# Kernel tuning notes

Hardware: AMD Instinct MI355X
Metric: run time of the kernel (lower is better)

Reference implementation:

```python
import jax, jax.numpy as jnp
import numpy as np


def _rel_pos_table(size, rel_pos):
    # q_size == k_size, fixed_input_size=True -> no interpolation, lambda=1
    coords = jnp.arange(size)[:, None] - jnp.arange(size)[None, :] + (size - 1)
    return rel_pos[coords]  # (size, size, head_dim)


def setup_inputs() -> dict:
    key = jax.random.key(0)
    ks = jax.random.split(key, 7)
    N, H, W, C = 8, 32, 32, 768
    hd = C // 12
    return {
        "x": jax.random.normal(ks[0], (N, H, W, C), jnp.float32),
        "w_qkv": jax.random.normal(ks[1], (C, 3 * C), jnp.float32) * 0.02,
        "b_qkv": jax.random.normal(ks[2], (3 * C,), jnp.float32) * 0.02,
        "w_proj": jax.random.normal(ks[3], (C, C), jnp.float32) * 0.02,
        "b_proj": jax.random.normal(ks[4], (C,), jnp.float32) * 0.02,
        "rel_pos_h": jax.random.normal(ks[5], (2 * H - 1, hd), jnp.float32) * 0.02,
        "rel_pos_w": jax.random.normal(ks[6], (2 * W - 1, hd), jnp.float32) * 0.02,
        "nb_heads": 12,
    }


def reference(x, w_qkv, b_qkv, w_proj, b_proj, rel_pos_h, rel_pos_w, nb_heads):
    N, H, W, C = x.shape
    hd = C // nb_heads
    scale = hd ** -0.5
    HW = H * W

    qkv = x.reshape(N, HW, C) @ w_qkv + b_qkv            # (N, HW, 3C)
    qkv = qkv.reshape(N, HW, 3, nb_heads, hd)
    qkv = jnp.transpose(qkv, (2, 0, 3, 1, 4)).reshape(3, N * nb_heads, HW, hd)
    q, k, v = qkv[0], qkv[1], qkv[2]

    attn = jnp.einsum('bqd,bkd->bqk', q, k) * scale      # (N*heads, HW, HW)

    # decomposed relative position bias (MViTv2)
    r_h = _rel_pos_table(H, rel_pos_h)                   # (H, H, hd)
    r_w = _rel_pos_table(W, rel_pos_w)                   # (W, W, hd)
    q4 = q.reshape(N * nb_heads, H, W, hd)
    bias_h = jnp.einsum('nhwc,hkc->nhwk', q4, r_h)       # (B, H, W, H)
    bias_w = jnp.einsum('nhwc,wkc->nhwk', q4, r_w)       # (B, H, W, W)
    attn = attn.reshape(N * nb_heads, H, W, H, W)
    attn = attn + bias_h[..., :, None] + bias_w[..., None, :]
    attn = attn.reshape(N * nb_heads, HW, HW)

    attn = jax.nn.softmax(attn, axis=-1)
    out = jnp.einsum('bqk,bkd->bqd', attn, v)            # (N*heads, HW, hd)
    out = out.reshape(N, nb_heads, H, W, hd)
    out = jnp.transpose(out, (0, 2, 3, 1, 4)).reshape(N, H, W, C)
    return out @ w_proj + b_proj
```

## Files before the change

kernel.cpp:

```cpp
#include <hip/hip_runtime.h>
#include <hip/hip_bf16.h>

#define N_    8
#define H_    32
#define W_    32
#define C_    768
#define NH_   12
#define HD_   64
#define B_    96
#define HW_   1024
#define C3_   2304
#define SCALE_ 0.125f
#define LOG2E_ 1.4426950408889634f

typedef __attribute__((ext_vector_type(4))) float f32x4;
typedef __attribute__((ext_vector_type(16))) float f32x16;
typedef __attribute__((ext_vector_type(8))) short s16x8;
typedef __attribute__((ext_vector_type(2))) int i32x2;
typedef __attribute__((ext_vector_type(2))) unsigned int u32x2;
typedef __attribute__((ext_vector_type(4))) unsigned int u32x4;
typedef unsigned short u16;
typedef unsigned int u32;

__device__ inline u16 f2b(float x) {
    __hip_bfloat16 h = __float2bfloat16(x);
    return *reinterpret_cast<u16*>(&h);
}
__device__ inline float b2f(u16 x) {
    u32 u = ((u32)x) << 16;
    return *reinterpret_cast<float*>(&u);
}
__device__ __forceinline__ u32 cvtpk(float a, float b) {
    u32 r;
    asm("v_cvt_pk_bf16_f32 %0, %1, %2" : "=v"(r) : "v"(a), "v"(b));
    return r;
}

__device__ __forceinline__ void gld_lds16(const void* g, void* l) {
    __builtin_amdgcn_global_load_lds(
        (const __attribute__((address_space(1))) u32*)g,
        (__attribute__((address_space(3))) u32*)l, 16, 0, 0);
}

__global__ __launch_bounds__(256) void cvt_bf16(const float* __restrict__ in,
                                                u16* __restrict__ out, int n4) {
    for (int i = blockIdx.x * blockDim.x + threadIdx.x; i < n4; i += gridDim.x * blockDim.x) {
        float4 v = ((const float4*)in)[i];
        ushort4 o;
        o.x = f2b(v.x); o.y = f2b(v.y); o.z = f2b(v.z); o.w = f2b(v.w);
        ((ushort4*)out)[i] = o;
    }
}

__global__ __launch_bounds__(256) void tcvt_bf16(const float* __restrict__ in,
                                                 u16* __restrict__ out, int K, int N) {
    __shared__ u16 tile[64][72];
    const int t = threadIdx.x;
    const int k0 = blockIdx.y * 64, n0 = blockIdx.x * 64;
    const int r = t >> 2, c4 = (t & 3) * 16;
    #pragma unroll
    for (int u = 0; u < 4; ++u) {
        float4 v = *(const float4*)(in + (size_t)(k0 + r) * N + n0 + c4 + u * 4);
        tile[c4 + u*4 + 0][r] = f2b(v.x);
        tile[c4 + u*4 + 1][r] = f2b(v.y);
        tile[c4 + u*4 + 2][r] = f2b(v.z);
        tile[c4 + u*4 + 3][r] = f2b(v.w);
    }
    __syncthreads();
    #pragma unroll
    for (int u = 0; u < 2; ++u) {
        s16x8 v;
        #pragma unroll
        for (int e = 0; e < 8; ++e) v[e] = (short)tile[r][c4 + u*8 + e];
        *(s16x8*)(out + (size_t)(n0 + r) * K + k0 + c4 + u*8) = v;
    }
}

#define G3_ISSUE(KB, BUF)                                                            \
    gld_lds16(gA0 + (KB), sAb + (BUF) * 4096 + w * 512);                             \
    gld_lds16(gA1 + (KB), sAb + (BUF) * 4096 + (w + 4) * 512);                       \
    gld_lds16(gB0 + (KB), sBb + (BUF) * 4096 + w * 512);                             \
    gld_lds16(gB1 + (KB), sBb + (BUF) * 4096 + (w + 4) * 512);

#define G3_COMP(BUF)                                                                 \
    {                                                                                \
        const u16* pa = sAb + (BUF) * 4096 + (wm * 64 + l15) * 32 + lg * 8;          \
        const u16* pb = sBb + (BUF) * 4096 + (wn * 64 + l15) * 32 + lg * 8;          \
        s16x8 afr[4], bfr[4];                                                        \
        _Pragma("unroll")                                                            \
        for (int i = 0; i < 4; ++i) {                                                \
            afr[i] = *(const s16x8*)(pa + i * 512);                                  \
            bfr[i] = *(const s16x8*)(pb + i * 512);                                  \
        }                                                                            \
        _Pragma("unroll")                                                            \
        for (int i = 0; i < 4; ++i)                                                  \
            _Pragma("unroll")                                                        \
            for (int j = 0; j < 4; ++j)                                              \
                acc[i][j] = __builtin_amdgcn_mfma_f32_16x16x32_bf16(afr[i], bfr[j],  \
                                                                    acc[i][j], 0, 0, 0); \
    }

#define G3_BAR4                                                                      \
    asm volatile("s_waitcnt vmcnt(4) lgkmcnt(0)" ::: "memory");                      \
    __builtin_amdgcn_s_barrier();                                                    \
    __builtin_amdgcn_sched_barrier(0);

#define G3_BAR0                                                                      \
    asm volatile("s_waitcnt vmcnt(0) lgkmcnt(0)" ::: "memory");                      \
    __builtin_amdgcn_s_barrier();                                                    \
    __builtin_amdgcn_sched_barrier(0);

#define GEMM_CORE3(A_, Bt_, NT_)                                                     \
    extern __shared__ char smem[];                                                   \
    u16* sAb = (u16*)smem;                                     \
    u16* sBb = (u16*)(smem + 24576);                           \
    const int t = threadIdx.x;                                                       \
    const int lane = t & 63;                                                         \
    const int w = t >> 6;                                                            \
    const int wm = w >> 1, wn = w & 1;                                               \
    const int l15 = lane & 15, lg = lane >> 4;                                       \
    const int per = (int)gridDim.x >> 3;                                             \
    const int swz = ((int)blockIdx.x & 7) * per + ((int)blockIdx.x >> 3);            \
    const int nbase = (swz % (NT_)) * 128;                                           \
    const int mbase = (swz / (NT_)) * 128;                                           \
    const int srow = lane >> 2;                                                      \
    const int sslot = lane & 3;                                                      \
    const u16* gA0 = (A_) + (size_t)(mbase + w * 16 + srow) * 768 + sslot * 8;       \
    const u16* gA1 = gA0 + (size_t)64 * 768;                                         \
    const u16* gB0 = (Bt_) + (size_t)(nbase + w * 16 + srow) * 768 + sslot * 8;      \
    const u16* gB1 = gB0 + (size_t)64 * 768;                                         \
    f32x4 acc[4][4] = {};                                                            \
    G3_ISSUE(0, 0)                                                                   \
    G3_ISSUE(32, 1)                                                                  \
    G3_BAR4                                                                          \
    for (int k3 = 0; k3 < 7; ++k3) {                                                 \
        const int kb = k3 * 96;                                                      \
        G3_ISSUE(kb + 64, 2)  G3_COMP(0)  G3_BAR4                                    \
        G3_ISSUE(kb + 96, 0)  G3_COMP(1)  G3_BAR4                                    \
        G3_ISSUE(kb + 128, 1) G3_COMP(2)  G3_BAR4                                    \
    }                                                                                \
    G3_ISSUE(736, 2) G3_COMP(0) G3_BAR4                                              \
    G3_COMP(1) G3_BAR0                                                               \
    G3_COMP(2) G3_BAR0

__global__ __launch_bounds__(256) void gemm_qkv(const u16* __restrict__ A,
                                                const u16* __restrict__ Bt,
                                                const float* __restrict__ bias,
                                                u16* __restrict__ qout,
                                                u16* __restrict__ kout,
                                                u16* __restrict__ vout) {
    GEMM_CORE3(A, Bt, 18)
    u16* T = (u16*)smem;

    const int which = nbase / C_;
    const int head0 = (nbase % C_) >> 6;
    const int n_img = mbase >> 10;
    const int pbase = mbase & 1023;

    if (which < 2) {
        #pragma unroll
        for (int i = 0; i < 4; ++i)
            #pragma unroll
            for (int r = 0; r < 4; ++r) {
                const int lm = wm * 64 + i * 16 + lg * 4 + r;
                #pragma unroll
                for (int j = 0; j < 4; ++j) {
                    const int lc = wn * 64 + j * 16 + l15;
                    T[lm * 136 + lc] = f2b(acc[i][j][r] + bias[nbase + lc]);
                }
            }
    } else {
        #pragma unroll
        for (int i = 0; i < 4; ++i)
            #pragma unroll
            for (int r = 0; r < 4; ++r) {
                const int lm = wm * 64 + i * 16 + lg * 4 + r;
                #pragma unroll
                for (int j = 0; j < 4; ++j) {
                    const int lc = wn * 64 + j * 16 + l15;
                    T[lc * 136 + lm] = f2b(acc[i][j][r] + bias[nbase + lc]);
                }
            }
    }
    __syncthreads();

    if (which < 2) {
        u16* dst = (which == 0) ? qout : kout;
        #pragma unroll
        for (int pass = 0; pass < 4; ++pass) {
            const int lm = pass * 32 + (t >> 3);
            #pragma unroll
            for (int hh = 0; hh < 2; ++hh) {
                s16x8 row = *(const s16x8*)(T + lm * 136 + hh * 64 + (t & 7) * 8);
                const size_t bidx = (size_t)(n_img * NH_ + head0 + hh);
                *(s16x8*)(dst + (bidx * HW_ + pbase + lm) * HD_ + (t & 7) * 8) = row;
            }
        }
    } else {
        #pragma unroll
        for (int pass = 0; pass < 8; ++pass) {
            const int lc = pass * 16 + (t >> 4);
            s16x8 row = *(const s16x8*)(T + lc * 136 + (t & 15) * 8);
            const int hh = lc >> 6, d = lc & 63;
            const size_t bidx = (size_t)(n_img * NH_ + head0 + hh);
            *(s16x8*)(vout + bidx * (size_t)(HW_ * HD_) + (size_t)d * HW_ + pbase + (t & 15) * 8) = row;
        }
    }
}

__global__ __launch_bounds__(256) void gemm_proj(const u16* __restrict__ A,
                                                 const u16* __restrict__ Bt,
                                                 const float* __restrict__ bias,
                                                 float* __restrict__ out) {
    GEMM_CORE3(A, Bt, 6)
    const int mrow0 = mbase + wm * 64 + lg * 4;
    #pragma unroll
    for (int i = 0; i < 4; ++i) {
        #pragma unroll
        for (int r = 0; r < 4; ++r) {
            const int m = mrow0 + i * 16 + r;
            #pragma unroll
            for (int j = 0; j < 4; ++j) {
                const int n = nbase + wn * 64 + j * 16 + l15;
                out[(size_t)m * C_ + n] = acc[i][j][r] + bias[n];
            }
        }
    }
}

__global__ __launch_bounds__(256) void ef_gemm(const u16* __restrict__ qb_,
                                               const float* __restrict__ rel_h,
                                               const float* __restrict__ rel_w,
                                               u16* __restrict__ Fg,
                                               u16* __restrict__ Eg) {
    const int t = threadIdx.x;
    const int lane = t & 63;
    const int w = t >> 6;
    const int l31 = lane & 31;
    const int hi  = lane >> 5;
    const size_t Mrow = (size_t)blockIdx.x * 128 + w * 32 + l31;

    s16x8 qb[4];
    {
        const u16* qrow = qb_ + Mrow * HD_;
        #pragma unroll
        for (int ck = 0; ck < 4; ++ck)
            qb[ck] = *(const s16x8*)(qrow + ck * 16 + hi * 8);
    }

    #pragma unroll
    for (int tb = 0; tb < 2; ++tb) {
        const float* R = tb ? rel_w : rel_h;
        u16* og = (tb ? Eg : Fg) + Mrow * 64;
        #pragma unroll
        for (int hh = 0; hh < 2; ++hh) {
            const int dr = hh * 32 + l31;
            const float* rrow = R + (size_t)(dr > 62 ? 62 : dr) * HD_;
            f32x16 acc = {};
            #pragma unroll
            for (int ck = 0; ck < 4; ++ck) {
                float4 r0 = *(const float4*)(rrow + ck * 16 + hi * 8);
                float4 r1 = *(const float4*)(rrow + ck * 16 + hi * 8 + 4);
                s16x8 af;
                af[0] = (short)f2b(r0.x * LOG2E_); af[1] = (short)f2b(r0.y * LOG2E_);
                af[2] = (short)f2b(r0.z * LOG2E_); af[3] = (short)f2b(r0.w * LOG2E_);
                af[4] = (short)f2b(r1.x * LOG2E_); af[5] = (short)f2b(r1.y * LOG2E_);
                af[6] = (short)f2b(r1.z * LOG2E_); af[7] = (short)f2b(r1.w * LOG2E_);
                acc = __builtin_amdgcn_mfma_f32_32x32x16_bf16(af, qb[ck], acc, 0, 0, 0);
            }
            #pragma unroll
            for (int u = 0; u < 4; ++u) {
                u32x2 pkd;
                pkd.x = cvtpk(acc[4*u+0], acc[4*u+1]);
                pkd.y = cvtpk(acc[4*u+2], acc[4*u+3]);
                *(u32x2*)(og + hh * 32 + u * 8 + 4 * hi) = pkd;
            }
        }
    }
}

__global__ __launch_bounds__(256) void attn_mfma(const u16* __restrict__ qb_,
                                                 const u16* __restrict__ kbf,
                                                 const u16* __restrict__ vtb,
                                                 const u16* __restrict__ Fg,
                                                 const u16* __restrict__ Eg,
                                                 u16* __restrict__ ob) {
    extern __shared__ char smem[];
    u16*   sBH  = (u16*)smem;
    u16*   sK0  = (u16*)(smem + 8704);
    u16*   sK1  = (u16*)(smem + 17920);
    u16*   sVt0 = (u16*)(smem + 27136);
    u16*   sVt1 = (u16*)(smem + 36352);

    const int t = threadIdx.x;
    const int lane = t & 63;
    const int w = t >> 6;
    const int l31 = lane & 31;
    const int hi  = lane >> 5;
    const int qw  = w * 32;

    const int bid = blockIdx.x;
    const int swz = (bid & 7) * 96 + (bid >> 3);
    const int b = swz >> 3;
    const int qbase = (swz & 7) * 128;

    s16x8 qfr[4];
    {
        const u16* qrow = qb_ + ((size_t)b * HW_ + qbase + qw + l31) * HD_;
        #pragma unroll
        for (int ck = 0; ck < 4; ++ck) {
            s16x8 qv = *(const s16x8*)(qrow + ck * 16 + hi * 8);
            #pragma unroll
            for (int e = 0; e < 8; ++e)
                qfr[ck][e] = (short)f2b(b2f((u16)qv[e]) * (SCALE_ * LOG2E_));
        }
    }

    {
        const u16* Fb = Fg + (size_t)b * HW_ * 64;
        for (int idv = t; idv < 4096; idv += 256) {
            const int row = idv >> 5;
            const int kh  = idv & 31;
            const int qg  = qbase + row;
            sBH[row * 34 + kh] = Fb[(size_t)qg * 64 + (qg >> 5) + 31 - kh];
        }
    }

    f32x4 bwv[4];
    {
        const int qmy = qbase + qw + l31;
        const u16* Erow = Eg + (size_t)(b * HW_ + qmy) * 64;
        #pragma unroll
        for (int m = 0; m < 4; ++m)
            #pragma unroll
            for (int j = 0; j < 4; ++j)
                bwv[m][j] = b2f(Erow[l31 + 31 - (m * 8 + 4 * hi + j)]);
    }

    const int srow = t >> 2;
    const int sc0  = (t & 3) * 16;
    const u16* kg = kbf + ((size_t)b * HW_ + srow) * HD_ + sc0;
    const u16* vg = vtb + (size_t)b * HD_ * HW_ + (size_t)srow * HW_ + sc0;
    u16* skw0 = sK0  + srow * 72 + sc0;
    u16* skw1 = sK1  + srow * 72 + sc0;
    u16* svw0 = sVt0 + srow * 72 + sc0;
    u16* svw1 = sVt1 + srow * 72 + sc0;

    s16x8 kr0 = *(const s16x8*)(kg);
    s16x8 kr1 = *(const s16x8*)(kg + 8);
    s16x8 vr0 = *(const s16x8*)(vg);
    s16x8 vr1 = *(const s16x8*)(vg + 8);
    *(s16x8*)(skw0)     = kr0;
    *(s16x8*)(skw0 + 8) = kr1;
    *(s16x8*)(svw0)     = vr0;
    *(s16x8*)(svw0 + 8) = vr1;
    __syncthreads();

    f32x16 Oacc[2] = {};
    f32x16 Osum = {};
    const u32x4 onesu = {0x3F803F80u, 0x3F803F80u, 0x3F803F80u, 0x3F803F80u};
    const s16x8 ones = *reinterpret_cast<const s16x8*>(&onesu);
    const int bhbase = (qw + l31) * 34;

    auto body = [&](int kt, const u16* sKr, const u16* sVr, u16* skwN, u16* svwN) {
        if (kt < 15) {
            const u16* kn = kg + (size_t)(kt + 1) * 64 * HD_;
            kr0 = *(const s16x8*)(kn);
            kr1 = *(const s16x8*)(kn + 8);
            const u16* vn = vg + (size_t)(kt + 1) * 64;
            vr0 = *(const s16x8*)(vn);
            vr1 = *(const s16x8*)(vn + 8);
        }

        const float bh0 = b2f(sBH[bhbase + 2 * kt]);
        const float bh1 = b2f(sBH[bhbase + 2 * kt + 1]);

        #pragma unroll
        for (int kvt = 0; kvt < 2; ++kvt) {
            f32x16 s = {};
            __builtin_amdgcn_s_setprio(1);
            #pragma unroll
            for (int ck = 0; ck < 4; ++ck) {
                s16x8 kf = *(const s16x8*)(sKr + (kvt * 32 + l31) * 72 + ck * 16 + hi * 8);
                s = __builtin_amdgcn_mfma_f32_32x32x16_bf16(kf, qfr[ck], s, 0, 0, 0);
            }
            __builtin_amdgcn_s_setprio(0);
            const float bh = kvt ? bh1 : bh0;

            u32 pw[8];
            #pragma unroll
            for (int m = 0; m < 8; ++m) {
                float p0 = __builtin_amdgcn_exp2f(s[2*m]   + bh + bwv[(2*m)>>2][(2*m)&3]);
                float p1 = __builtin_amdgcn_exp2f(s[2*m+1] + bh + bwv[(2*m+1)>>2][(2*m+1)&3]);
                pw[m] = cvtpk(p0, p1);
            }

            __builtin_amdgcn_s_setprio(1);
            #pragma unroll
            for (int cc = 0; cc < 2; ++cc) {
                i32x2 s02 = __builtin_amdgcn_permlane32_swap((int)pw[cc*4+0], (int)pw[cc*4+2], false, false);
                i32x2 s13 = __builtin_amdgcn_permlane32_swap((int)pw[cc*4+1], (int)pw[cc*4+3], false, false);
                u32x4 pau;
                pau.x = (u32)s02.x; pau.y = (u32)s13.x;
                pau.z = (u32)s02.y; pau.w = (u32)s13.y;
                s16x8 pa = *reinterpret_cast<s16x8*>(&pau);
                const int kc = kvt * 2 + cc;
                #pragma unroll
                for (int dt = 0; dt < 2; ++dt) {
                    s16x8 vf = *(const s16x8*)(sVr + (dt * 32 + l31) * 72 + kc * 16 + hi * 8);
                    Oacc[dt] = __builtin_amdgcn_mfma_f32_32x32x16_bf16(pa, vf, Oacc[dt], 0, 0, 0);
                }
                Osum = __builtin_amdgcn_mfma_f32_32x32x16_bf16(pa, ones, Osum, 0, 0, 0);
            }
            __builtin_amdgcn_s_setprio(0);
        }

        if (kt < 15) {
            *(s16x8*)(skwN)     = kr0;
            *(s16x8*)(skwN + 8) = kr1;
            *(s16x8*)(svwN)     = vr0;
            *(s16x8*)(svwN + 8) = vr1;
        }
        asm volatile("s_waitcnt lgkmcnt(0)" ::: "memory");
        __builtin_amdgcn_s_barrier();
        __builtin_amdgcn_sched_barrier(0);
    };

    for (int k2 = 0; k2 < 8; ++k2) {
        body(2 * k2,     sK0, sVt0, skw1, svw1);
        body(2 * k2 + 1, sK1, sVt1, skw0, svw0);
    }

    const int n_img = b / NH_;
    const int head  = b % NH_;
    #pragma unroll
    for (int dt = 0; dt < 2; ++dt) {
        #pragma unroll
        for (int r = 0; r < 16; ++r) {
            const int qloc = (r & 3) + 8 * (r >> 2) + 4 * hi;
            const int qg = qbase + qw + qloc;
            ob[(size_t)(n_img * HW_ + qg) * C_ + head * HD_ + dt * 32 + l31] =
                f2b(Oacc[dt][r] / Osum[r]);
        }
    }
}

extern "C" void kernel_launch(void* const* d_in, const int* in_sizes, int n_in,
                              void* d_out, int out_size, void* d_ws, size_t ws_size,
                              hipStream_t stream) {
    const float* x      = (const float*)d_in[0];
    const float* w_qkv  = (const float*)d_in[1];
    const float* b_qkv  = (const float*)d_in[2];
    const float* w_proj = (const float*)d_in[3];
    const float* b_proj = (const float*)d_in[4];
    const float* rel_h  = (const float*)d_in[5];
    const float* rel_w  = (const float*)d_in[6];
    float* out = (float*)d_out;

    const size_t seg = (size_t)B_ * HW_ * HD_;
    char* p = (char*)d_ws;
    u16* xb     = (u16*)p;  p += seg * 2;
    u16* wqkvT  = (u16*)p;  p += (size_t)C3_ * C_ * 2;
    u16* wprojT = (u16*)p;  p += (size_t)C_ * C_ * 2;
    u16* qb     = (u16*)p;  p += seg * 2;
    u16* kbf    = (u16*)p;  p += seg * 2;
    u16* vtb    = (u16*)p;  p += seg * 2;
    u16* ob     = (u16*)p;  p += seg * 2;
    u16* Fg     = (u16*)p;  p += seg * 2;
    u16* Eg     = (u16*)p;  p += seg * 2;

    cvt_bf16<<<2048, 256, 0, stream>>>(x, xb, (int)(seg / 4));
    tcvt_bf16<<<dim3(C3_ / 64, C_ / 64), 256, 0, stream>>>(w_qkv, wqkvT, C_, C3_);
    tcvt_bf16<<<dim3(C_ / 64, C_ / 64), 256, 0, stream>>>(w_proj, wprojT, C_, C_);

    gemm_qkv<<<1152, 256, 49152, stream>>>(xb, wqkvT, b_qkv, qb, kbf, vtb);
    ef_gemm<<<768, 256, 0, stream>>>(qb, rel_h, rel_w, Fg, Eg);
    attn_mfma<<<768, 256, 45568, stream>>>(qb, kbf, vtb, Fg, Eg, ob);
    gemm_proj<<<384, 256, 49152, stream>>>(ob, wprojT, b_proj, out);
}
```

Baseline: 141.1 us.

## Use 32x32x16 MFMA in QKV/proj GEMMs and remap tiles per XCD

Replaces the 16x16x32 bf16 MFMA tiling in the shared GEMM core with 32x32x16 MFMAs. Each wave now computes a 2x2 grid of 32x32 accumulators, which cuts the number of LDS fragment reads per MFMA and the instruction count. The epilogues are rewritten to match the 32x32 accumulator register layout. The block-to-tile swizzle is also replaced with an explicit XCD-aware mapping, so each XCD works on a contiguous M/N region and L2 reuse improves. The new mapping hardcodes the grid shape and makes the lane-to-row mapping more intricate, which raises the risk of mistakes.

```diff
diff --git a/kernel.cpp b/kernel.cpp
--- a/kernel.cpp
+++ b/kernel.cpp
@@ -84,20 +84,24 @@
 
 #define G3_COMP(BUF)                                                                 \
     {                                                                                \
-        const u16* pa = sAb + (BUF) * 4096 + (wm * 64 + l15) * 32 + lg * 8;          \
-        const u16* pb = sBb + (BUF) * 4096 + (wn * 64 + l15) * 32 + lg * 8;          \
-        s16x8 afr[4], bfr[4];                                                        \
+        const u16* pa = sAb + (BUF) * 4096 + (wm * 64 + l31) * 32 + hi * 8;          \
+        const u16* pb = sBb + (BUF) * 4096 + (wn * 64 + l31) * 32 + hi * 8;          \
+        s16x8 afr[2][2], bfr[2][2];                                                  \
         _Pragma("unroll")                                                            \
-        for (int i = 0; i < 4; ++i) {                                                \
-            afr[i] = *(const s16x8*)(pa + i * 512);                                  \
-            bfr[i] = *(const s16x8*)(pb + i * 512);                                  \
-        }                                                                            \
+        for (int mi = 0; mi < 2; ++mi)                                               \
+            _Pragma("unroll")                                                        \
+            for (int kc = 0; kc < 2; ++kc) {                                         \
+                afr[mi][kc] = *(const s16x8*)(pa + mi * 1024 + kc * 16);             \
+                bfr[mi][kc] = *(const s16x8*)(pb + mi * 1024 + kc * 16);             \
+            }                                                                        \
         _Pragma("unroll")                                                            \
-        for (int i = 0; i < 4; ++i)                                                  \
+        for (int mi = 0; mi < 2; ++mi)                                               \
             _Pragma("unroll")                                                        \
-            for (int j = 0; j < 4; ++j)                                              \
-                acc[i][j] = __builtin_amdgcn_mfma_f32_16x16x32_bf16(afr[i], bfr[j],  \
-                                                                    acc[i][j], 0, 0, 0); \
+            for (int nj = 0; nj < 2; ++nj)                                           \
+                _Pragma("unroll")                                                    \
+                for (int kc = 0; kc < 2; ++kc)                                       \
+                    acc[mi][nj] = __builtin_amdgcn_mfma_f32_32x32x16_bf16(           \
+                        afr[mi][kc], bfr[nj][kc], acc[mi][nj], 0, 0, 0);             \
     }
 
 #define G3_BAR4                                                                      \
@@ -110,7 +114,7 @@
     __builtin_amdgcn_s_barrier();                                                    \
     __builtin_amdgcn_sched_barrier(0);
 
-#define GEMM_CORE3(A_, Bt_, NT_)                                                     \
+#define GEMM_CORE3(A_, Bt_)                                                          \
     extern __shared__ char smem[];                                                   \
     u16* sAb = (u16*)smem;                                     \
     u16* sBb = (u16*)(smem + 24576);                           \
@@ -118,18 +122,14 @@
     const int lane = t & 63;                                                         \
     const int w = t >> 6;                                                            \
     const int wm = w >> 1, wn = w & 1;                                               \
-    const int l15 = lane & 15, lg = lane >> 4;                                       \
-    const int per = (int)gridDim.x >> 3;                                             \
-    const int swz = ((int)blockIdx.x & 7) * per + ((int)blockIdx.x >> 3);            \
-    const int nbase = (swz % (NT_)) * 128;                                           \
-    const int mbase = (swz / (NT_)) * 128;                                           \
+    const int l31 = lane & 31, hi = lane >> 5;                                       \
     const int srow = lane >> 2;                                                      \
     const int sslot = lane & 3;                                                      \
     const u16* gA0 = (A_) + (size_t)(mbase + w * 16 + srow) * 768 + sslot * 8;       \
     const u16* gA1 = gA0 + (size_t)64 * 768;                                         \
     const u16* gB0 = (Bt_) + (size_t)(nbase + w * 16 + srow) * 768 + sslot * 8;      \
     const u16* gB1 = gB0 + (size_t)64 * 768;                                         \
-    f32x4 acc[4][4] = {};                                                            \
+    f32x16 acc[2][2] = {};                                                           \
     G3_ISSUE(0, 0)                                                                   \
     G3_ISSUE(32, 1)                                                                  \
     G3_BAR4                                                                          \
@@ -149,7 +149,11 @@
                                                 u16* __restrict__ qout,
                                                 u16* __restrict__ kout,
                                                 u16* __restrict__ vout) {
-    GEMM_CORE3(A, Bt, 18)
+    const int xcd = blockIdx.x & 7;
+    const int local = blockIdx.x >> 3;
+    const int mbase = (((xcd >> 1) << 4) + (local & 15)) * 128;
+    const int nbase = ((xcd & 1) * 9 + (local >> 4)) * 128;
+    GEMM_CORE3(A, Bt)
     u16* T = (u16*)smem;
 
     const int which = nbase / C_;
@@ -159,28 +163,26 @@
 
     if (which < 2) {
         #pragma unroll
-        for (int i = 0; i < 4; ++i)
-            #pragma unroll
-            for (int r = 0; r < 4; ++r) {
-                const int lm = wm * 64 + i * 16 + lg * 4 + r;
+        for (int mi = 0; mi < 2; ++mi)
+            #pragma unroll
+            for (int nj = 0; nj < 2; ++nj)
                 #pragma unroll
-                for (int j = 0; j < 4; ++j) {
-                    const int lc = wn * 64 + j * 16 + l15;
-                    T[lm * 136 + lc] = f2b(acc[i][j][r] + bias[nbase + lc]);
+                for (int r = 0; r < 16; ++r) {
+                    const int lm = wm * 64 + mi * 32 + ((r & 3) + 8 * (r >> 2) + 4 * hi);
+                    const int lc = wn * 64 + nj * 32 + l31;
+                    T[lm * 136 + lc] = f2b(acc[mi][nj][r] + bias[nbase + lc]);
                 }
-            }
     } else {
         #pragma unroll
-        for (int i = 0; i < 4; ++i)
-            #pragma unroll
-            for (int r = 0; r < 4; ++r) {
-                const int lm = wm * 64 + i * 16 + lg * 4 + r;
+        for (int mi = 0; mi < 2; ++mi)
+            #pragma unroll
+            for (int nj = 0; nj < 2; ++nj)
                 #pragma unroll
-                for (int j = 0; j < 4; ++j) {
-                    const int lc = wn * 64 + j * 16 + l15;
-                    T[lc * 136 + lm] = f2b(acc[i][j][r] + bias[nbase + lc]);
+                for (int r = 0; r < 16; ++r) {
+                    const int lm = wm * 64 + mi * 32 + ((r & 3) + 8 * (r >> 2) + 4 * hi);
+                    const int lc = wn * 64 + nj * 32 + l31;
+                    T[lc * 136 + lm] = f2b(acc[mi][nj][r] + bias[nbase + lc]);
                 }
-            }
     }
     __syncthreads();
 
@@ -212,20 +214,21 @@
                                                  const u16* __restrict__ Bt,
                                                  const float* __restrict__ bias,
                                                  float* __restrict__ out) {
-    GEMM_CORE3(A, Bt, 6)
-    const int mrow0 = mbase + wm * 64 + lg * 4;
+    const int xcd = blockIdx.x & 7;
+    const int local = blockIdx.x >> 3;
+    const int mbase = (xcd * 8 + (local & 7)) * 128;
+    const int nbase = (local >> 3) * 128;
+    GEMM_CORE3(A, Bt)
     #pragma unroll
-    for (int i = 0; i < 4; ++i) {
-        #pragma unroll
-        for (int r = 0; r < 4; ++r) {
-            const int m = mrow0 + i * 16 + r;
-            #pragma unroll
-            for (int j = 0; j < 4; ++j) {
-                const int n = nbase + wn * 64 + j * 16 + l15;
-                out[(size_t)m * C_ + n] = acc[i][j][r] + bias[n];
-            }
-        }
-    }
+    for (int mi = 0; mi < 2; ++mi)
+        #pragma unroll
+        for (int nj = 0; nj < 2; ++nj)
+            #pragma unroll
+            for (int r = 0; r < 16; ++r) {
+                const int m = mbase + wm * 64 + mi * 32 + ((r & 3) + 8 * (r >> 2) + 4 * hi);
+                const int n = nbase + wn * 64 + nj * 32 + l31;
+                out[(size_t)m * C_ + n] = acc[mi][nj][r] + bias[n];
+            }
 }
 
 __global__ __launch_bounds__(256) void ef_gemm(const u16* __restrict__ qb_,
```

After: 145.5 us. 3.1% more time.

## Fuse rel-pos bias GEMM into QKV epilogue and merge prep conversion kernels

Applied to the files above, without the earlier changes.

Merges the x conversion and both weight transpose-conversions into one launch with a block-index split. The separate ef_gemm kernel is removed. Its rel-pos projection now runs in the gemm_qkv epilogue for Q tiles, reading Q from shared memory instead of re-reading it from global. This drops two launches and one global read of Q. In exchange, Q-tile blocks get extra epilogue work, which makes block runtimes uneven and may raise register pressure.

```diff
diff --git a/kernel.cpp b/kernel.cpp
--- a/kernel.cpp
+++ b/kernel.cpp
@@ -42,21 +42,31 @@
         (__attribute__((address_space(3))) u32*)l, 16, 0, 0);
 }
 
-__global__ __launch_bounds__(256) void cvt_bf16(const float* __restrict__ in,
-                                                u16* __restrict__ out, int n4) {
-    for (int i = blockIdx.x * blockDim.x + threadIdx.x; i < n4; i += gridDim.x * blockDim.x) {
-        float4 v = ((const float4*)in)[i];
-        ushort4 o;
-        o.x = f2b(v.x); o.y = f2b(v.y); o.z = f2b(v.z); o.w = f2b(v.w);
-        ((ushort4*)out)[i] = o;
-    }
-}
-
-__global__ __launch_bounds__(256) void tcvt_bf16(const float* __restrict__ in,
-                                                 u16* __restrict__ out, int K, int N) {
+__global__ __launch_bounds__(256) void prep_fused(const float* __restrict__ x,
+                                                  u16* __restrict__ xb,
+                                                  const float* __restrict__ w_qkv,
+                                                  u16* __restrict__ wqkvT,
+                                                  const float* __restrict__ w_proj,
+                                                  u16* __restrict__ wprojT) {
     __shared__ u16 tile[64][72];
     const int t = threadIdx.x;
-    const int k0 = blockIdx.y * 64, n0 = blockIdx.x * 64;
+    const int bid = blockIdx.x;
+    if (bid < 2048) {
+        const int n4 = (int)((size_t)B_ * HW_ * HD_ / 4);
+        for (int i = bid * 256 + t; i < n4; i += 2048 * 256) {
+            float4 v = ((const float4*)x)[i];
+            ushort4 o;
+            o.x = f2b(v.x); o.y = f2b(v.y); o.z = f2b(v.z); o.w = f2b(v.w);
+            ((ushort4*)xb)[i] = o;
+        }
+        return;
+    }
+    int rem = bid - 2048;
+    const float* in;
+    u16* outp;
+    int N, n0, k0;
+    if (rem < 432) { in = w_qkv;  outp = wqkvT;  N = C3_; n0 = (rem % 36) * 64; k0 = (rem / 36) * 64; }
+    else { rem -= 432; in = w_proj; outp = wprojT; N = C_;  n0 = (rem % 12) * 64; k0 = (rem / 12) * 64; }
     const int r = t >> 2, c4 = (t & 3) * 16;
     #pragma unroll
     for (int u = 0; u < 4; ++u) {
@@ -72,7 +82,7 @@
         s16x8 v;
         #pragma unroll
         for (int e = 0; e < 8; ++e) v[e] = (short)tile[r][c4 + u*8 + e];
-        *(s16x8*)(out + (size_t)(n0 + r) * K + k0 + c4 + u*8) = v;
+        *(s16x8*)(outp + (size_t)(n0 + r) * 768 + k0 + c4 + u*8) = v;
     }
 }
 
@@ -146,9 +156,13 @@
 __global__ __launch_bounds__(256) void gemm_qkv(const u16* __restrict__ A,
                                                 const u16* __restrict__ Bt,
                                                 const float* __restrict__ bias,
+                                                const float* __restrict__ rel_h,
+                                                const float* __restrict__ rel_w,
                                                 u16* __restrict__ qout,
                                                 u16* __restrict__ kout,
-                                                u16* __restrict__ vout) {
+                                                u16* __restrict__ vout,
+                                                u16* __restrict__ Fg,
+                                                u16* __restrict__ Eg) {
     GEMM_CORE3(A, Bt, 18)
     u16* T = (u16*)smem;
 
@@ -204,6 +218,49 @@
             const int hh = lc >> 6, d = lc & 63;
             const size_t bidx = (size_t)(n_img * NH_ + head0 + hh);
             *(s16x8*)(vout + bidx * (size_t)(HW_ * HD_) + (size_t)d * HW_ + pbase + (t & 15) * 8) = row;
+        }
+    }
+
+    if (which == 0) {
+        const int l31e = lane & 31;
+        const int hie  = lane >> 5;
+        #pragma unroll
+        for (int hh2 = 0; hh2 < 2; ++hh2) {
+            s16x8 qfe[4];
+            #pragma unroll
+            for (int ck = 0; ck < 4; ++ck)
+                qfe[ck] = *(const s16x8*)(T + (w * 32 + l31e) * 136 + hh2 * 64 + ck * 16 + hie * 8);
+            const size_t rowbase =
+                ((size_t)(n_img * NH_ + head0 + hh2) * HW_ + pbase + w * 32 + l31e) * 64;
+            #pragma unroll
+            for (int tb = 0; tb < 2; ++tb) {
+                const float* R = tb ? rel_w : rel_h;
+                u16* og = (tb ? Eg : Fg) + rowbase;
+                #pragma unroll
+                for (int hh = 0; hh < 2; ++hh) {
+                    const int dr = hh * 32 + l31e;
+                    const float* rrow = R + (size_t)(dr > 62 ? 62 : dr) * HD_;
+                    f32x16 acce = {};
+                    #pragma unroll
+                    for (int ck = 0; ck < 4; ++ck) {
+                        float4 r0 = *(const float4*)(rrow + ck * 16 + hie * 8);
+                        float4 r1 = *(const float4*)(rrow + ck * 16 + hie * 8 + 4);
+                        s16x8 af;
+                        af[0] = (short)f2b(r0.x * LOG2E_); af[1] = (short)f2b(r0.y * LOG2E_);
+                        af[2] = (short)f2b(r0.z * LOG2E_); af[3] = (short)f2b(r0.w * LOG2E_);
+                        af[4] = (short)f2b(r1.x * LOG2E_); af[5] = (short)f2b(r1.y * LOG2E_);
+                        af[6] = (short)f2b(r1.z * LOG2E_); af[7] = (short)f2b(r1.w * LOG2E_);
+                        acce = __builtin_amdgcn_mfma_f32_32x32x16_bf16(af, qfe[ck], acce, 0, 0, 0);
+                    }
+                    #pragma unroll
+                    for (int u = 0; u < 4; ++u) {
+                        u32x2 pkd;
+                        pkd.x = cvtpk(acce[4*u+0], acce[4*u+1]);
+                        pkd.y = cvtpk(acce[4*u+2], acce[4*u+3]);
+                        *(u32x2*)(og + hh * 32 + u * 8 + 4 * hie) = pkd;
+                    }
+                }
+            }
         }
     }
 }
@@ -223,57 +280,6 @@
             for (int j = 0; j < 4; ++j) {
                 const int n = nbase + wn * 64 + j * 16 + l15;
                 out[(size_t)m * C_ + n] = acc[i][j][r] + bias[n];
-            }
-        }
-    }
-}
-
-__global__ __launch_bounds__(256) void ef_gemm(const u16* __restrict__ qb_,
-                                               const float* __restrict__ rel_h,
-                                               const float* __restrict__ rel_w,
-                                               u16* __restrict__ Fg,
-                                               u16* __restrict__ Eg) {
-    const int t = threadIdx.x;
-    const int lane = t & 63;
-    const int w = t >> 6;
-    const int l31 = lane & 31;
-    const int hi  = lane >> 5;
-    const size_t Mrow = (size_t)blockIdx.x * 128 + w * 32 + l31;
-
-    s16x8 qb[4];
-    {
-        const u16* qrow = qb_ + Mrow * HD_;
-        #pragma unroll
-        for (int ck = 0; ck < 4; ++ck)
-            qb[ck] = *(const s16x8*)(qrow + ck * 16 + hi * 8);
-    }
-
-    #pragma unroll
-    for (int tb = 0; tb < 2; ++tb) {
-        const float* R = tb ? rel_w : rel_h;
-        u16* og = (tb ? Eg : Fg) + Mrow * 64;
-        #pragma unroll
-        for (int hh = 0; hh < 2; ++hh) {
-            const int dr = hh * 32 + l31;
-            const float* rrow = R + (size_t)(dr > 62 ? 62 : dr) * HD_;
-            f32x16 acc = {};
-            #pragma unroll
-            for (int ck = 0; ck < 4; ++ck) {
-                float4 r0 = *(const float4*)(rrow + ck * 16 + hi * 8);
-                float4 r1 = *(const float4*)(rrow + ck * 16 + hi * 8 + 4);
-                s16x8 af;
-                af[0] = (short)f2b(r0.x * LOG2E_); af[1] = (short)f2b(r0.y * LOG2E_);
-                af[2] = (short)f2b(r0.z * LOG2E_); af[3] = (short)f2b(r0.w * LOG2E_);
-                af[4] = (short)f2b(r1.x * LOG2E_); af[5] = (short)f2b(r1.y * LOG2E_);
-                af[6] = (short)f2b(r1.z * LOG2E_); af[7] = (short)f2b(r1.w * LOG2E_);
-                acc = __builtin_amdgcn_mfma_f32_32x32x16_bf16(af, qb[ck], acc, 0, 0, 0);
-            }
-            #pragma unroll
-            for (int u = 0; u < 4; ++u) {
-                u32x2 pkd;
-                pkd.x = cvtpk(acc[4*u+0], acc[4*u+1]);
-                pkd.y = cvtpk(acc[4*u+2], acc[4*u+3]);
-                *(u32x2*)(og + hh * 32 + u * 8 + 4 * hi) = pkd;
             }
         }
     }
@@ -469,12 +475,9 @@
     u16* Fg     = (u16*)p;  p += seg * 2;
     u16* Eg     = (u16*)p;  p += seg * 2;
 
-    cvt_bf16<<<2048, 256, 0, stream>>>(x, xb, (int)(seg / 4));
-    tcvt_bf16<<<dim3(C3_ / 64, C_ / 64), 256, 0, stream>>>(w_qkv, wqkvT, C_, C3_);
-    tcvt_bf16<<<dim3(C_ / 64, C_ / 64), 256, 0, stream>>>(w_proj, wprojT, C_, C_);
-
-    gemm_qkv<<<1152, 256, 49152, stream>>>(xb, wqkvT, b_qkv, qb, kbf, vtb);
-    ef_gemm<<<768, 256, 0, stream>>>(qb, rel_h, rel_w, Fg, Eg);
+    prep_fused<<<2624, 256, 0, stream>>>(x, xb, w_qkv, wqkvT, w_proj, wprojT);
+    gemm_qkv<<<1152, 256, 49152, stream>>>(xb, wqkvT, b_qkv, rel_h, rel_w,
+                                           qb, kbf, vtb, Fg, Eg);
     attn_mfma<<<768, 256, 45568, stream>>>(qb, kbf, vtb, Fg, Eg, ob);
     gemm_proj<<<384, 256, 49152, stream>>>(ob, wprojT, b_proj, out);
 }
```

New measurement: 138.3 us. -2.0%, faster.
